# Kernel tuning notes

Measured on AMD Instinct MI355X. Metric: run time of the kernel, lower is better.

Reference implementation:

```python
import jax, jax.numpy as jnp
import numpy as np

N = 100000
E = 1600000
D_IN = 128
D_HID = 32
NEG_SLOPE = 0.2


def _glorot(key, shape):
    fan_in, fan_out = shape[0], shape[-1]
    lim = jnp.sqrt(6.0 / (fan_in + fan_out))
    return jax.random.uniform(key, shape, jnp.float32, -lim, lim)


def setup_inputs() -> dict:
    key = jax.random.key(0)
    ks = jax.random.split(key, 10)
    x = jax.random.normal(ks[0], (N, D_IN), jnp.float32)
    edge_index = jax.random.randint(ks[1], (2, E), 0, N, jnp.int64)
    return {
        "x": x,
        "edge_index": edge_index,
        "W1_l": _glorot(ks[2], (D_IN, D_HID)),
        "W1_r": _glorot(ks[3], (D_IN, D_HID)),
        "att1": _glorot(ks[4], (D_HID,)),
        "b1": jnp.zeros((D_HID,), jnp.float32),
        "W2_l": _glorot(ks[5], (D_HID, D_HID)),
        "W2_r": _glorot(ks[6], (D_HID, D_HID)),
        "att2": _glorot(ks[7], (D_HID,)),
        "b2": jnp.zeros((D_HID,), jnp.float32),
    }


def _segment_softmax(logits, seg, num_segments):
    m = jax.ops.segment_max(logits, seg, num_segments=num_segments)
    m = jnp.where(jnp.isfinite(m), m, 0.0)
    ex = jnp.exp(logits - m[seg])
    s = jax.ops.segment_sum(ex, seg, num_segments=num_segments)
    return ex / (s[seg] + 1e-16)


def _gatv2(x, edge_index, W_l, W_r, att, b):
    # GATv2Conv, heads=1, add_self_loops=False, share_weights=False
    src, dst = edge_index[0], edge_index[1]
    x_l = x @ W_l  # source transform [N, D_HID]
    x_r = x @ W_r  # target transform [N, D_HID]
    # per-edge attention logit: att . leaky_relu(x_l[j] + x_r[i])
    h = x_l[src] + x_r[dst]  # [E, D_HID]
    e = jnp.where(h > 0, h, NEG_SLOPE * h) @ att  # [E]
    alpha = _segment_softmax(e, dst, x.shape[0])  # softmax over incoming edges
    out = jax.ops.segment_sum(alpha[:, None] * x_l[src], dst,
                              num_segments=x.shape[0])
    return out + b


def reference(x, edge_index, W1_l, W1_r, att1, b1, W2_l, W2_r, att2, b2):
    h = _gatv2(x, edge_index, W1_l, W1_r, att1, b1)
    h = jax.nn.relu(h)
    return _gatv2(h, edge_index, W2_l, W2_r, att2, b2)
```

## Files before the change

kernel.cpp:

```cpp
#include <hip/hip_runtime.h>
#include <hip/hip_bf16.h>

#define D_HID 32
#define D_IN 128
#define NEG 0.2f
#define BSH 7
#define BSZ 128
#define MAXB 1024

typedef unsigned short u16;
typedef __attribute__((ext_vector_type(8))) short short8;
typedef __attribute__((ext_vector_type(4))) float float4v;

__device__ __forceinline__ float b2f(u16 u){
  union { unsigned int i; float f; } c; c.i = ((unsigned int)u) << 16; return c.f;
}

__device__ __forceinline__ u16 f2b_rne(float f){
  union { float f; unsigned int u; } c; c.f = f;
  unsigned int u = c.u;
  return (u16)((u + 0x7FFFu + ((u >> 16) & 1u)) >> 16);
}

__device__ __forceinline__ void split_bf16(float v, u16& hi, u16& lo){
  hi = f2b_rne(v);
  lo = f2b_rne(v - b2f(hi));
}

__device__ __forceinline__ float ldf(const void* __restrict__ p, int f32, long long i){
  return f32 ? ((const float*)p)[i] : b2f(((const u16*)p)[i]);
}

__device__ __forceinline__ int atomAddI(int* p, int v){
  return __hip_atomic_fetch_add(p, v, __ATOMIC_RELAXED, __HIP_MEMORY_SCOPE_AGENT);
}

__global__ void detect_flags(const int* __restrict__ ei, const u16* __restrict__ xw,
                             int* __restrict__ flags){
  __shared__ int insane_s, nz_s;
  int t = threadIdx.x;
  if (t == 0){ insane_s = 0; nz_s = 0; }
  __syncthreads();
  int pred = (t < 64) ? (ei[2*t+1] != 0) : 0;
  int e = (xw[t] >> 7) & 0xFF;
  int bad = (e < 100 || e > 140) ? 1 : 0;
  #pragma unroll
  for (int off = 32; off >= 1; off >>= 1){
    bad  += __shfl_down(bad,  off, 64);
    pred += __shfl_down(pred, off, 64);
  }
  if ((t & 63) == 0){
    atomicAdd(&insane_s, bad);
    atomicAdd(&nz_s, pred);
  }
  __syncthreads();
  if (t == 0){
    flags[0] = (nz_s == 0) ? 1 : 0;
    flags[1] = (insane_s > 16) ? 1 : 0;
  }
}

__device__ __forceinline__ void edge_nodes(const int* __restrict__ ei, int E_, int is64,
                                           int e, int& src, int& dst){
  if (is64){ src = ei[2*e]; dst = ei[2*E_ + 2*e]; }
  else     { src = ei[e];   dst = ei[E_ + e]; }
}

__global__ void prep_wfrag(const void* __restrict__ Wl, const void* __restrict__ Wr,
                           const int* __restrict__ flags, int K,
                           uint4* __restrict__ whi, uint4* __restrict__ wlo){
  int t = blockIdx.x * blockDim.x + threadIdx.x;
  int KS = K >> 5;
  int total = 4 * KS * 64;
  if (t >= total) return;
  int lane = t & 63;
  int rem = t >> 6;
  int kstep = rem % KS;
  int ctile = rem / KS;
  int f32 = flags[1];
  int col = ctile * 16 + (lane & 15);
  int quad = lane >> 4;
  union { u16 s[8]; uint4 q; } ch, cl;
  #pragma unroll
  for (int j = 0; j < 8; ++j){
    int k = kstep*32 + quad*8 + j;
    float v = (col < 32) ? ldf(Wl, f32, (long long)k*D_HID + col)
                         : ldf(Wr, f32, (long long)k*D_HID + (col - 32));
    u16 hi, lo; split_bf16(v, hi, lo);
    ch.s[j] = hi; cl.s[j] = lo;
  }
  whi[rem*64 + lane] = ch.q;
  wlo[rem*64 + lane] = cl.q;
}

template<int K>
__global__ void mfma_gemm(const void* __restrict__ X,
                          const uint4* __restrict__ whi, const uint4* __restrict__ wlo,
                          const int* __restrict__ flags, int force_f32,
                          float* __restrict__ xl, float* __restrict__ xr, int N_)
{
  constexpr int KS = K >> 5;
  int tile = blockIdx.x * (blockDim.x >> 6) + (threadIdx.x >> 6);
  if (tile * 16 >= N_) return;
  int lane = threadIdx.x & 63;
  int quad = lane >> 4;
  int m = tile*16 + (lane & 15);
  if (m >= N_) m = N_ - 1;
  int f32 = force_f32 | flags[1];

  float4v acc[4];
  #pragma unroll
  for (int c = 0; c < 4; ++c) acc[c] = (float4v){0.f,0.f,0.f,0.f};

  #pragma unroll
  for (int ks = 0; ks < KS; ++ks){
    long long base = (long long)m * K + ks*32 + quad*8;
    float av[8];
    if (f32){
      const float4* xp = (const float4*)((const float*)X + base);
      float4 t0 = xp[0], t1 = xp[1];
      av[0]=t0.x; av[1]=t0.y; av[2]=t0.z; av[3]=t0.w;
      av[4]=t1.x; av[5]=t1.y; av[6]=t1.z; av[7]=t1.w;
    } else {
      union { uint4 q; u16 s[8]; } c8;
      c8.q = *(const uint4*)((const u16*)X + base);
      #pragma unroll
      for (int j = 0; j < 8; ++j) av[j] = b2f(c8.s[j]);
    }
    short8 ahi, alo;
    #pragma unroll
    for (int j = 0; j < 8; ++j){
      u16 hi, lo; split_bf16(av[j], hi, lo);
      ahi[j] = (short)hi; alo[j] = (short)lo;
    }
    #pragma unroll
    for (int c = 0; c < 4; ++c){
      uint4 wh = whi[(c*KS + ks)*64 + lane];
      uint4 wl = wlo[(c*KS + ks)*64 + lane];
      short8 bh = *(short8*)&wh;
      short8 bl = *(short8*)&wl;
      acc[c] = __builtin_amdgcn_mfma_f32_16x16x32_bf16(ahi, bh, acc[c], 0, 0, 0);
      acc[c] = __builtin_amdgcn_mfma_f32_16x16x32_bf16(ahi, bl, acc[c], 0, 0, 0);
      acc[c] = __builtin_amdgcn_mfma_f32_16x16x32_bf16(alo, bh, acc[c], 0, 0, 0);
    }
  }

  #pragma unroll
  for (int c = 0; c < 4; ++c){
    int col = c*16 + (lane & 15);
    float* dst = (col < 32) ? xl : xr;
    int kk = col & 31;
    #pragma unroll
    for (int r = 0; r < 4; ++r){
      int node = tile*16 + quad*4 + r;
      if (node < N_) dst[(size_t)node*D_HID + kk] = acc[c][r];
    }
  }
}

__global__ void bucket_count(const int* __restrict__ ei, const int* __restrict__ flags,
                             int* __restrict__ gcnt, int E_, int B_){
  __shared__ int hist[MAXB];
  for (int i = threadIdx.x; i < B_; i += 256) hist[i] = 0;
  __syncthreads();
  int chunk = (E_ + gridDim.x - 1) / gridDim.x;
  int s = blockIdx.x * chunk;
  int e = s + chunk; if (e > E_) e = E_;
  int is64 = flags[0];
  for (int i = s + (int)threadIdx.x; i < e; i += 256){
    int dst = is64 ? ei[2*E_ + 2*i] : ei[E_ + i];
    atomicAdd(&hist[dst >> BSH], 1);
  }
  __syncthreads();
  for (int i = threadIdx.x; i < B_; i += 256)
    if (hist[i]) (void)atomAddI(&gcnt[i], hist[i]);
}

__global__ void scan_buckets(const int* __restrict__ gcnt, int* __restrict__ offsets,
                             int* __restrict__ cursor, int B_){
  __shared__ int sd[1024];
  int t = threadIdx.x;
  int v = (t < B_) ? gcnt[t] : 0;
  sd[t] = v;
  __syncthreads();
  for (int off = 1; off < 1024; off <<= 1){
    int tmp = (t >= off) ? sd[t-off] : 0;
    __syncthreads();
    sd[t] += tmp;
    __syncthreads();
  }
  if (t < B_){
    int excl = sd[t] - v;
    offsets[t] = excl;
    cursor[t]  = excl;
    if (t == B_-1) offsets[B_] = sd[t];
  }
}

__global__ void bucket_scatter(const int* __restrict__ ei, const int* __restrict__ flags,
                               int* __restrict__ cursor, unsigned* __restrict__ seg,
                               int E_, int B_){
  __shared__ int hist[MAXB];
  __shared__ int bbase[MAXB];
  for (int i = threadIdx.x; i < B_; i += 256) hist[i] = 0;
  __syncthreads();
  int chunk = (E_ + gridDim.x - 1) / gridDim.x;
  int s = blockIdx.x * chunk;
  int e = s + chunk; if (e > E_) e = E_;
  int is64 = flags[0];
  for (int i = s + (int)threadIdx.x; i < e; i += 256){
    int dst = is64 ? ei[2*E_ + 2*i] : ei[E_ + i];
    atomicAdd(&hist[dst >> BSH], 1);
  }
  __syncthreads();
  for (int i = threadIdx.x; i < B_; i += 256){
    int c = hist[i];
    bbase[i] = c ? atomAddI(&cursor[i], c) : 0;
  }
  __syncthreads();
  for (int i = threadIdx.x; i < B_; i += 256) hist[i] = 0;
  __syncthreads();
  for (int i = s + (int)threadIdx.x; i < e; i += 256){
    int src, dst;
    edge_nodes(ei, E_, is64, i, src, dst);
    int b = dst >> BSH;
    int pos = bbase[b] + atomicAdd(&hist[b], 1);
    seg[pos] = ((unsigned)src << BSH) | (unsigned)(dst & (BSZ-1));
  }
}

__global__ void bucket_finalize(const unsigned* __restrict__ seg,
                                const int* __restrict__ offsets,
                                int* __restrict__ row, int* __restrict__ csr_src,
                                int N_, int B_){
  __shared__ int hist[BSZ];
  __shared__ int sc[BSZ];
  __shared__ int loff[BSZ];
  int b = blockIdx.x;
  int t = threadIdx.x;
  int base = offsets[b], cnt = offsets[b+1] - base;
  if (t < BSZ) hist[t] = 0;
  __syncthreads();
  for (int i = t; i < cnt; i += 256)
    atomicAdd(&hist[seg[base+i] & (BSZ-1)], 1);
  __syncthreads();
  if (t < BSZ) sc[t] = hist[t];
  __syncthreads();
  for (int off = 1; off < BSZ; off <<= 1){
    int tmp = (t < BSZ && t >= off) ? sc[t-off] : 0;
    __syncthreads();
    if (t < BSZ) sc[t] += tmp;
    __syncthreads();
  }
  if (t < BSZ){
    int excl = sc[t] - hist[t];
    loff[t] = excl;
    int node = b*BSZ + t;
    if (node <= N_) row[node] = base + excl;
  }
  if (b == B_-1 && t == 0) row[N_] = offsets[B_];
  __syncthreads();
  for (int i = t; i < cnt; i += 256){
    unsigned en = seg[base+i];
    int dl = en & (BSZ-1);
    int pos = atomicAdd(&loff[dl], 1);
    csr_src[base + pos] = (int)en;
  }
}

__global__ void gat_gather(const int* __restrict__ row, const unsigned* __restrict__ csrp,
                           const float* __restrict__ xl, const float* __restrict__ xr,
                           const void* __restrict__ att, const void* __restrict__ bias,
                           const int* __restrict__ flags,
                           float* __restrict__ outp, int N_, int do_relu)
{
  int G = (blockIdx.x * blockDim.x + threadIdx.x) >> 3;
  if (G >= N_) return;
  int fl = threadIdx.x & 7;
  int f32 = flags[1];
  float4 attk;
  attk.x = ldf(att, f32, fl*4+0);
  attk.y = ldf(att, f32, fl*4+1);
  attk.z = ldf(att, f32, fl*4+2);
  attk.w = ldf(att, f32, fl*4+3);
  int n = G;
  float4 xrk = *(const float4*)(xr + (size_t)n*D_HID + fl*4);
  int rs = row[n], re = row[n+1];
  const char* xlb = (const char*)xl;
  unsigned fo = (unsigned)(fl << 4);

  unsigned enB = 0;
  float4 xlA = make_float4(0.f, 0.f, 0.f, 0.f);
  if (rs < re){
    unsigned enA = csrp[rs];
    if (rs + 1 < re) enB = csrp[rs+1];
    xlA = *(const float4*)(xlb + (enA & ~127u) + fo);
  }

  float4 acc = make_float4(0.f, 0.f, 0.f, 0.f);
  float ssum = 0.f;
  for (int i = rs; i < re; ++i){
    float4 xv = xlA;
    unsigned enN = enB;
    if (i + 2 < re) enB = csrp[i+2];
    if (i + 1 < re) xlA = *(const float4*)(xlb + (enN & ~127u) + fo);
    float4 hh;
    hh.x = xv.x + xrk.x; hh.x = fmaxf(hh.x, NEG*hh.x);
    hh.y = xv.y + xrk.y; hh.y = fmaxf(hh.y, NEG*hh.y);
    hh.z = xv.z + xrk.z; hh.z = fmaxf(hh.z, NEG*hh.z);
    hh.w = xv.w + xrk.w; hh.w = fmaxf(hh.w, NEG*hh.w);
    float p = hh.x*attk.x;
    p = fmaf(hh.y, attk.y, p);
    p = fmaf(hh.z, attk.z, p);
    p = fmaf(hh.w, attk.w, p);
    p += __shfl_xor(p, 1, 8);
    p += __shfl_xor(p, 2, 8);
    p += __shfl_xor(p, 4, 8);
    p = fminf(p, 60.f);
    float ev = __expf(p);
    ssum += ev;
    acc.x = fmaf(ev, xv.x, acc.x);
    acc.y = fmaf(ev, xv.y, acc.y);
    acc.z = fmaf(ev, xv.z, acc.z);
    acc.w = fmaf(ev, xv.w, acc.w);
  }

  float inv = 1.0f / (ssum + 1e-16f);
  float4 o;
  o.x = acc.x*inv + ldf(bias, f32, fl*4+0);
  o.y = acc.y*inv + ldf(bias, f32, fl*4+1);
  o.z = acc.z*inv + ldf(bias, f32, fl*4+2);
  o.w = acc.w*inv + ldf(bias, f32, fl*4+3);
  if (do_relu){
    o.x = fmaxf(o.x, 0.f); o.y = fmaxf(o.y, 0.f);
    o.z = fmaxf(o.z, 0.f); o.w = fmaxf(o.w, 0.f);
  }
  *(float4*)(outp + (size_t)n*D_HID + fl*4) = o;
}

extern "C" void kernel_launch(void* const* d_in, const int* in_sizes, int n_in,
                              void* d_out, int out_size, void* d_ws, size_t ws_size,
                              hipStream_t stream)
{
  const void* x   = d_in[0];
  const int*  ei  = (const int*)d_in[1];
  const void* W1l = d_in[2];
  const void* W1r = d_in[3];
  const void* att1= d_in[4];
  const void* b1  = d_in[5];
  const void* W2l = d_in[6];
  const void* W2r = d_in[7];
  const void* att2= d_in[8];
  const void* b2  = d_in[9];
  float* out = (float*)d_out;

  int N_ = in_sizes[0] / D_IN;
  int E_ = in_sizes[1] / 2;
  int B_ = (N_ + BSZ - 1) / BSZ;

  char* ws = (char*)d_ws;
  size_t off = 0;
  auto carve = [&](size_t bytes) -> char* {
    char* p = ws + off;
    off += (bytes + 255) & ~(size_t)255;
    return p;
  };
  float*    xl      = (float*)   carve((size_t)N_ * D_HID * 4);
  float*    xr      = (float*)   carve((size_t)N_ * D_HID * 4);
  float*    h       = (float*)   carve((size_t)N_ * D_HID * 4);
  unsigned* seg     = (unsigned*)carve((size_t)E_ * 4);
  int*      csr_src = (int*)     carve((size_t)E_ * 4);
  int*      row     = (int*)     carve((size_t)(N_ + 1) * 4);
  int*      offsets = (int*)     carve((size_t)(MAXB + 1) * 4);
  int*      gcnt    = (int*)     carve((size_t)MAXB * 4);
  int*      cursor  = (int*)     carve((size_t)MAXB * 4);
  int*      flags   = (int*)     carve(256);
  uint4*    whi1    = (uint4*)   carve((size_t)4 * 4 * 64 * 16);
  uint4*    wlo1    = (uint4*)   carve((size_t)4 * 4 * 64 * 16);
  uint4*    whi2    = (uint4*)   carve((size_t)4 * 1 * 64 * 16);
  uint4*    wlo2    = (uint4*)   carve((size_t)4 * 1 * 64 * 16);

  const int tpb = 256;
  int gG = (N_ + 31) / 32;
  int tiles = (N_ + 15) / 16;
  int gT = (tiles + 3) / 4;

  detect_flags<<<1, 256, 0, stream>>>(ei, (const u16*)x, flags);

  prep_wfrag<<<4, 256, 0, stream>>>(W1l, W1r, flags, D_IN, whi1, wlo1);
  prep_wfrag<<<1, 256, 0, stream>>>(W2l, W2r, flags, D_HID, whi2, wlo2);

  hipMemsetAsync(gcnt, 0, (size_t)MAXB * 4, stream);
  bucket_count<<<256, tpb, 0, stream>>>(ei, flags, gcnt, E_, B_);
  scan_buckets<<<1, 1024, 0, stream>>>(gcnt, offsets, cursor, B_);
  bucket_scatter<<<256, tpb, 0, stream>>>(ei, flags, cursor, seg, E_, B_);
  bucket_finalize<<<B_, tpb, 0, stream>>>(seg, offsets, row, csr_src, N_, B_);

  mfma_gemm<D_IN><<<gT, tpb, 0, stream>>>(x, whi1, wlo1, flags, 0, xl, xr, N_);
  gat_gather<<<gG, tpb, 0, stream>>>(row, (const unsigned*)csr_src, xl, xr,
                                     att1, b1, flags, h, N_, 1);

  mfma_gemm<D_HID><<<gT, tpb, 0, stream>>>(h, whi2, wlo2, flags, 1, xl, xr, N_);
  gat_gather<<<gG, tpb, 0, stream>>>(row, (const unsigned*)csr_src, xl, xr,
                                     att2, b2, flags, out, N_, 0);
}
```

Measured before the change: 270.9 us.

## Sort nodes by in-degree for gather balance and deepen edge prefetch

```diff
diff --git a/kernel.cpp b/kernel.cpp
--- a/kernel.cpp
+++ b/kernel.cpp
@@ -7,6 +7,7 @@
 #define BSH 7
 #define BSZ 128
 #define MAXB 1024
+#define MAXD 128
 
 typedef unsigned short u16;
 typedef __attribute__((ext_vector_type(8))) short short8;
@@ -33,6 +34,31 @@
 
 __device__ __forceinline__ int atomAddI(int* p, int v){
   return __hip_atomic_fetch_add(p, v, __ATOMIC_RELAXED, __HIP_MEMORY_SCOPE_AGENT);
+}
+
+__device__ __forceinline__ float red8(float p){
+  p += __int_as_float(__builtin_amdgcn_update_dpp(
+         0, __float_as_int(p), 0xB1, 0xF, 0xF, true));
+  p += __int_as_float(__builtin_amdgcn_update_dpp(
+         0, __float_as_int(p), 0x4E, 0xF, 0xF, true));
+  p += __int_as_float(__builtin_amdgcn_ds_swizzle(
+         __float_as_int(p), 0x101F));
+  return p;
+}
+
+__device__ __forceinline__ float edge_ev(const float4 xv, const float4 xrk,
+                                         const float4 attk){
+  float hx = xv.x + xrk.x; hx = fmaxf(hx, NEG*hx);
+  float hy = xv.y + xrk.y; hy = fmaxf(hy, NEG*hy);
+  float hz = xv.z + xrk.z; hz = fmaxf(hz, NEG*hz);
+  float hw = xv.w + xrk.w; hw = fmaxf(hw, NEG*hw);
+  float p = hx*attk.x;
+  p = fmaf(hy, attk.y, p);
+  p = fmaf(hz, attk.z, p);
+  p = fmaf(hw, attk.w, p);
+  p = red8(p);
+  p = fminf(p, 60.f);
+  return __expf(p);
 }
 
 __global__ void detect_flags(const int* __restrict__ ei, const u16* __restrict__ xw,
@@ -232,19 +258,26 @@
 __global__ void bucket_finalize(const unsigned* __restrict__ seg,
                                 const int* __restrict__ offsets,
                                 int* __restrict__ row, int* __restrict__ csr_src,
+                                int* __restrict__ dhist,
                                 int N_, int B_){
   __shared__ int hist[BSZ];
   __shared__ int sc[BSZ];
   __shared__ int loff[BSZ];
+  __shared__ int dh[MAXD];
   int b = blockIdx.x;
   int t = threadIdx.x;
   int base = offsets[b], cnt = offsets[b+1] - base;
   if (t < BSZ) hist[t] = 0;
+  if (t < MAXD) dh[t] = 0;
   __syncthreads();
   for (int i = t; i < cnt; i += 256)
     atomicAdd(&hist[seg[base+i] & (BSZ-1)], 1);
   __syncthreads();
-  if (t < BSZ) sc[t] = hist[t];
+  if (t < BSZ){
+    sc[t] = hist[t];
+    int node = b*BSZ + t;
+    if (node < N_) atomicAdd(&dh[min(hist[t], MAXD-1)], 1);
+  }
   __syncthreads();
   for (int off = 1; off < BSZ; off <<= 1){
     int tmp = (t < BSZ && t >= off) ? sc[t-off] : 0;
@@ -266,9 +299,56 @@
     int pos = atomicAdd(&loff[dl], 1);
     csr_src[base + pos] = (int)en;
   }
+  __syncthreads();
+  if (t < MAXD && dh[t]) (void)atomAddI(&dhist[t], dh[t]);
+}
+
+__global__ void scan_deg(const int* __restrict__ dhist, int* __restrict__ dcur){
+  __shared__ int sd[MAXD];
+  int t = threadIdx.x;
+  int v = dhist[t];
+  sd[t] = v;
+  __syncthreads();
+  for (int off = 1; off < MAXD; off <<= 1){
+    int tmp = (t >= off) ? sd[t-off] : 0;
+    __syncthreads();
+    sd[t] += tmp;
+    __syncthreads();
+  }
+  dcur[t] = sd[t] - v;
+}
+
+__global__ void deg_scatter(const int* __restrict__ row, int* __restrict__ dcur,
+                            int* __restrict__ perm, int N_){
+  __shared__ int h[MAXD];
+  __shared__ int base[MAXD];
+  int t = threadIdx.x;
+  int chunk = (N_ + gridDim.x - 1) / gridDim.x;
+  int s = blockIdx.x * chunk;
+  int e = s + chunk; if (e > N_) e = N_;
+  if (t < MAXD) h[t] = 0;
+  __syncthreads();
+  for (int n = s + t; n < e; n += 256){
+    int d = min(row[n+1] - row[n], MAXD-1);
+    atomicAdd(&h[d], 1);
+  }
+  __syncthreads();
+  if (t < MAXD){
+    int c = h[t];
+    base[t] = c ? atomAddI(&dcur[t], c) : 0;
+  }
+  __syncthreads();
+  if (t < MAXD) h[t] = 0;
+  __syncthreads();
+  for (int n = s + t; n < e; n += 256){
+    int d = min(row[n+1] - row[n], MAXD-1);
+    int pos = base[d] + atomicAdd(&h[d], 1);
+    perm[pos] = n;
+  }
 }
 
 __global__ void gat_gather(const int* __restrict__ row, const unsigned* __restrict__ csrp,
+                           const int* __restrict__ perm,
                            const float* __restrict__ xl, const float* __restrict__ xr,
                            const void* __restrict__ att, const void* __restrict__ bias,
                            const int* __restrict__ flags,
@@ -283,46 +363,48 @@
   attk.y = ldf(att, f32, fl*4+1);
   attk.z = ldf(att, f32, fl*4+2);
   attk.w = ldf(att, f32, fl*4+3);
-  int n = G;
+  int n = perm[G];
   float4 xrk = *(const float4*)(xr + (size_t)n*D_HID + fl*4);
   int rs = row[n], re = row[n+1];
   const char* xlb = (const char*)xl;
   unsigned fo = (unsigned)(fl << 4);
 
-  unsigned enB = 0;
-  float4 xlA = make_float4(0.f, 0.f, 0.f, 0.f);
-  if (rs < re){
-    unsigned enA = csrp[rs];
-    if (rs + 1 < re) enB = csrp[rs+1];
-    xlA = *(const float4*)(xlb + (enA & ~127u) + fo);
-  }
-
   float4 acc = make_float4(0.f, 0.f, 0.f, 0.f);
   float ssum = 0.f;
-  for (int i = rs; i < re; ++i){
-    float4 xv = xlA;
-    unsigned enN = enB;
-    if (i + 2 < re) enB = csrp[i+2];
-    if (i + 1 < re) xlA = *(const float4*)(xlb + (enN & ~127u) + fo);
-    float4 hh;
-    hh.x = xv.x + xrk.x; hh.x = fmaxf(hh.x, NEG*hh.x);
-    hh.y = xv.y + xrk.y; hh.y = fmaxf(hh.y, NEG*hh.y);
-    hh.z = xv.z + xrk.z; hh.z = fmaxf(hh.z, NEG*hh.z);
-    hh.w = xv.w + xrk.w; hh.w = fmaxf(hh.w, NEG*hh.w);
-    float p = hh.x*attk.x;
-    p = fmaf(hh.y, attk.y, p);
-    p = fmaf(hh.z, attk.z, p);
-    p = fmaf(hh.w, attk.w, p);
-    p += __shfl_xor(p, 1, 8);
-    p += __shfl_xor(p, 2, 8);
-    p += __shfl_xor(p, 4, 8);
-    p = fminf(p, 60.f);
-    float ev = __expf(p);
-    ssum += ev;
-    acc.x = fmaf(ev, xv.x, acc.x);
-    acc.y = fmaf(ev, xv.y, acc.y);
-    acc.z = fmaf(ev, xv.z, acc.z);
-    acc.w = fmaf(ev, xv.w, acc.w);
+
+  if (rs < re){
+    int last = re - 1;
+    unsigned c0 = csrp[rs];
+    unsigned c1 = csrp[min(rs+1, last)];
+    unsigned c2 = csrp[min(rs+2, last)];
+    unsigned c3 = csrp[min(rs+3, last)];
+    unsigned ca = csrp[min(rs+4, last)];
+    unsigned cb = csrp[min(rs+5, last)];
+    float4 xv0 = *(const float4*)(xlb + (c0 & ~127u) + fo);
+    float4 xv1 = *(const float4*)(xlb + (c1 & ~127u) + fo);
+    float4 xv2 = *(const float4*)(xlb + (c2 & ~127u) + fo);
+    float4 xv3 = *(const float4*)(xlb + (c3 & ~127u) + fo);
+    for (int i = rs; i < re; i += 2){
+      float4 nx0 = *(const float4*)(xlb + (ca & ~127u) + fo);
+      float4 nx1 = *(const float4*)(xlb + (cb & ~127u) + fo);
+      unsigned na = csrp[min(i+6, last)];
+      unsigned nb = csrp[min(i+7, last)];
+      float ev0 = edge_ev(xv0, xrk, attk);
+      ssum += ev0;
+      acc.x = fmaf(ev0, xv0.x, acc.x);
+      acc.y = fmaf(ev0, xv0.y, acc.y);
+      acc.z = fmaf(ev0, xv0.z, acc.z);
+      acc.w = fmaf(ev0, xv0.w, acc.w);
+      float ev1 = edge_ev(xv1, xrk, attk);
+      ev1 = (i + 1 <= last) ? ev1 : 0.f;
+      ssum += ev1;
+      acc.x = fmaf(ev1, xv1.x, acc.x);
+      acc.y = fmaf(ev1, xv1.y, acc.y);
+      acc.z = fmaf(ev1, xv1.z, acc.z);
+      acc.w = fmaf(ev1, xv1.w, acc.w);
+      xv0 = xv2; xv1 = xv3; xv2 = nx0; xv3 = nx1;
+      ca = na; cb = nb;
+    }
   }
 
   float inv = 1.0f / (ssum + 1e-16f);
@@ -371,9 +453,12 @@
   unsigned* seg     = (unsigned*)carve((size_t)E_ * 4);
   int*      csr_src = (int*)     carve((size_t)E_ * 4);
   int*      row     = (int*)     carve((size_t)(N_ + 1) * 4);
+  int*      perm    = (int*)     carve((size_t)N_ * 4);
   int*      offsets = (int*)     carve((size_t)(MAXB + 1) * 4);
   int*      gcnt    = (int*)     carve((size_t)MAXB * 4);
   int*      cursor  = (int*)     carve((size_t)MAXB * 4);
+  int*      dhist   = (int*)     carve((size_t)MAXD * 4);
+  int*      dcur    = (int*)     carve((size_t)MAXD * 4);
   int*      flags   = (int*)     carve(256);
   uint4*    whi1    = (uint4*)   carve((size_t)4 * 4 * 64 * 16);
   uint4*    wlo1    = (uint4*)   carve((size_t)4 * 4 * 64 * 16);
@@ -391,16 +476,20 @@
   prep_wfrag<<<1, 256, 0, stream>>>(W2l, W2r, flags, D_HID, whi2, wlo2);
 
   hipMemsetAsync(gcnt, 0, (size_t)MAXB * 4, stream);
+  hipMemsetAsync(dhist, 0, (size_t)MAXD * 4, stream);
   bucket_count<<<256, tpb, 0, stream>>>(ei, flags, gcnt, E_, B_);
   scan_buckets<<<1, 1024, 0, stream>>>(gcnt, offsets, cursor, B_);
   bucket_scatter<<<256, tpb, 0, stream>>>(ei, flags, cursor, seg, E_, B_);
-  bucket_finalize<<<B_, tpb, 0, stream>>>(seg, offsets, row, csr_src, N_, B_);
+  bucket_finalize<<<B_, tpb, 0, stream>>>(seg, offsets, row, csr_src, dhist, N_, B_);
+
+  scan_deg<<<1, MAXD, 0, stream>>>(dhist, dcur);
+  deg_scatter<<<64, tpb, 0, stream>>>(row, dcur, perm, N_);
 
   mfma_gemm<D_IN><<<gT, tpb, 0, stream>>>(x, whi1, wlo1, flags, 0, xl, xr, N_);
-  gat_gather<<<gG, tpb, 0, stream>>>(row, (const unsigned*)csr_src, xl, xr,
+  gat_gather<<<gG, tpb, 0, stream>>>(row, (const unsigned*)csr_src, perm, xl, xr,
                                      att1, b1, flags, h, N_, 1);
 
   mfma_gemm<D_HID><<<gT, tpb, 0, stream>>>(h, whi2, wlo2, flags, 1, xl, xr, N_);
-  gat_gather<<<gG, tpb, 0, stream>>>(row, (const unsigned*)csr_src, xl, xr,
+  gat_gather<<<gG, tpb, 0, stream>>>(row, (const unsigned*)csr_src, perm, xl, xr,
                                      att2, b2, flags, out, N_, 0);
 }
```

After: 275.9 us. Within noise of the previous version (+1.8%).

## Drop per-node CSR finalize; aggregate bucketed edges with LDS atomics

Applied to the files above, without the earlier changes.

```diff
diff --git a/kernel.cpp b/kernel.cpp
--- a/kernel.cpp
+++ b/kernel.cpp
@@ -7,6 +7,7 @@
 #define BSH 7
 #define BSZ 128
 #define MAXB 1024
+#define APAD 36
 
 typedef unsigned short u16;
 typedef __attribute__((ext_vector_type(8))) short short8;
@@ -33,6 +34,31 @@
 
 __device__ __forceinline__ int atomAddI(int* p, int v){
   return __hip_atomic_fetch_add(p, v, __ATOMIC_RELAXED, __HIP_MEMORY_SCOPE_AGENT);
+}
+
+__device__ __forceinline__ float red8(float p){
+  p += __int_as_float(__builtin_amdgcn_update_dpp(
+         0, __float_as_int(p), 0xB1, 0xF, 0xF, true));
+  p += __int_as_float(__builtin_amdgcn_update_dpp(
+         0, __float_as_int(p), 0x4E, 0xF, 0xF, true));
+  p += __int_as_float(__builtin_amdgcn_ds_swizzle(
+         __float_as_int(p), 0x101F));
+  return p;
+}
+
+__device__ __forceinline__ float edge_ev(const float4 xv, const float4 xrk,
+                                         const float4 attk){
+  float hx = xv.x + xrk.x; hx = fmaxf(hx, NEG*hx);
+  float hy = xv.y + xrk.y; hy = fmaxf(hy, NEG*hy);
+  float hz = xv.z + xrk.z; hz = fmaxf(hz, NEG*hz);
+  float hw = xv.w + xrk.w; hw = fmaxf(hw, NEG*hw);
+  float p = hx*attk.x;
+  p = fmaf(hy, attk.y, p);
+  p = fmaf(hz, attk.z, p);
+  p = fmaf(hw, attk.w, p);
+  p = red8(p);
+  p = fminf(p, 60.f);
+  return __expf(p);
 }
 
 __global__ void detect_flags(const int* __restrict__ ei, const u16* __restrict__ xw,
@@ -229,113 +255,110 @@
   }
 }
 
-__global__ void bucket_finalize(const unsigned* __restrict__ seg,
-                                const int* __restrict__ offsets,
-                                int* __restrict__ row, int* __restrict__ csr_src,
-                                int N_, int B_){
-  __shared__ int hist[BSZ];
-  __shared__ int sc[BSZ];
-  __shared__ int loff[BSZ];
+__global__ void __launch_bounds__(512)
+gat_edge(const unsigned* __restrict__ seg, const int* __restrict__ offsets,
+         const float* __restrict__ xl, const float* __restrict__ xr,
+         const void* __restrict__ att, const void* __restrict__ bias,
+         const int* __restrict__ flags,
+         float* __restrict__ outp, int N_, int do_relu)
+{
+  __shared__ float accs[BSZ][APAD];
+  __shared__ float xrs[BSZ][APAD];
   int b = blockIdx.x;
   int t = threadIdx.x;
-  int base = offsets[b], cnt = offsets[b+1] - base;
-  if (t < BSZ) hist[t] = 0;
-  __syncthreads();
-  for (int i = t; i < cnt; i += 256)
-    atomicAdd(&hist[seg[base+i] & (BSZ-1)], 1);
-  __syncthreads();
-  if (t < BSZ) sc[t] = hist[t];
-  __syncthreads();
-  for (int off = 1; off < BSZ; off <<= 1){
-    int tmp = (t < BSZ && t >= off) ? sc[t-off] : 0;
-    __syncthreads();
-    if (t < BSZ) sc[t] += tmp;
-    __syncthreads();
-  }
-  if (t < BSZ){
-    int excl = sc[t] - hist[t];
-    loff[t] = excl;
-    int node = b*BSZ + t;
-    if (node <= N_) row[node] = base + excl;
-  }
-  if (b == B_-1 && t == 0) row[N_] = offsets[B_];
-  __syncthreads();
-  for (int i = t; i < cnt; i += 256){
-    unsigned en = seg[base+i];
-    int dl = en & (BSZ-1);
-    int pos = atomicAdd(&loff[dl], 1);
-    csr_src[base + pos] = (int)en;
-  }
-}
-
-__global__ void gat_gather(const int* __restrict__ row, const unsigned* __restrict__ csrp,
-                           const float* __restrict__ xl, const float* __restrict__ xr,
-                           const void* __restrict__ att, const void* __restrict__ bias,
-                           const int* __restrict__ flags,
-                           float* __restrict__ outp, int N_, int do_relu)
-{
-  int G = (blockIdx.x * blockDim.x + threadIdx.x) >> 3;
-  if (G >= N_) return;
-  int fl = threadIdx.x & 7;
+  int fl = t & 7;
+  int g  = t >> 3;
+  int node0 = b * BSZ;
   int f32 = flags[1];
+
+  for (int i = t; i < BSZ*APAD; i += 512) ((float*)accs)[i] = 0.f;
+  for (int i = t; i < BSZ*8; i += 512){
+    int dl = i >> 3, fq = i & 7;
+    int node = node0 + dl;
+    float4 v = make_float4(0.f,0.f,0.f,0.f);
+    if (node < N_) v = *(const float4*)(xr + (size_t)node*D_HID + fq*4);
+    *(float4*)&xrs[dl][fq*4] = v;
+  }
+  __syncthreads();
+
   float4 attk;
   attk.x = ldf(att, f32, fl*4+0);
   attk.y = ldf(att, f32, fl*4+1);
   attk.z = ldf(att, f32, fl*4+2);
   attk.w = ldf(att, f32, fl*4+3);
-  int n = G;
-  float4 xrk = *(const float4*)(xr + (size_t)n*D_HID + fl*4);
-  int rs = row[n], re = row[n+1];
+
+  int base = offsets[b], cnt = offsets[b+1] - base;
   const char* xlb = (const char*)xl;
   unsigned fo = (unsigned)(fl << 4);
 
-  unsigned enB = 0;
-  float4 xlA = make_float4(0.f, 0.f, 0.f, 0.f);
-  if (rs < re){
-    unsigned enA = csrp[rs];
-    if (rs + 1 < re) enB = csrp[rs+1];
-    xlA = *(const float4*)(xlb + (enA & ~127u) + fo);
-  }
-
-  float4 acc = make_float4(0.f, 0.f, 0.f, 0.f);
-  float ssum = 0.f;
-  for (int i = rs; i < re; ++i){
-    float4 xv = xlA;
-    unsigned enN = enB;
-    if (i + 2 < re) enB = csrp[i+2];
-    if (i + 1 < re) xlA = *(const float4*)(xlb + (enN & ~127u) + fo);
-    float4 hh;
-    hh.x = xv.x + xrk.x; hh.x = fmaxf(hh.x, NEG*hh.x);
-    hh.y = xv.y + xrk.y; hh.y = fmaxf(hh.y, NEG*hh.y);
-    hh.z = xv.z + xrk.z; hh.z = fmaxf(hh.z, NEG*hh.z);
-    hh.w = xv.w + xrk.w; hh.w = fmaxf(hh.w, NEG*hh.w);
-    float p = hh.x*attk.x;
-    p = fmaf(hh.y, attk.y, p);
-    p = fmaf(hh.z, attk.z, p);
-    p = fmaf(hh.w, attk.w, p);
-    p += __shfl_xor(p, 1, 8);
-    p += __shfl_xor(p, 2, 8);
-    p += __shfl_xor(p, 4, 8);
-    p = fminf(p, 60.f);
-    float ev = __expf(p);
-    ssum += ev;
-    acc.x = fmaf(ev, xv.x, acc.x);
-    acc.y = fmaf(ev, xv.y, acc.y);
-    acc.z = fmaf(ev, xv.z, acc.z);
-    acc.w = fmaf(ev, xv.w, acc.w);
-  }
-
-  float inv = 1.0f / (ssum + 1e-16f);
-  float4 o;
-  o.x = acc.x*inv + ldf(bias, f32, fl*4+0);
-  o.y = acc.y*inv + ldf(bias, f32, fl*4+1);
-  o.z = acc.z*inv + ldf(bias, f32, fl*4+2);
-  o.w = acc.w*inv + ldf(bias, f32, fl*4+3);
-  if (do_relu){
-    o.x = fmaxf(o.x, 0.f); o.y = fmaxf(o.y, 0.f);
-    o.z = fmaxf(o.z, 0.f); o.w = fmaxf(o.w, 0.f);
-  }
-  *(float4*)(outp + (size_t)n*D_HID + fl*4) = o;
+  if (cnt > 0){
+    int chunk = (cnt + 63) >> 6;
+    int nit = (chunk + 1) >> 1;
+    int gs = base + g * chunk;
+    int ge = min(gs + chunk, base + cnt);
+    int last = base + cnt - 1;
+
+    unsigned c0 = seg[min(gs+0, last)];
+    unsigned c1 = seg[min(gs+1, last)];
+    unsigned c2 = seg[min(gs+2, last)];
+    unsigned c3 = seg[min(gs+3, last)];
+    float4 x0 = *(const float4*)(xlb + (c0 & ~127u) + fo);
+    float4 x1 = *(const float4*)(xlb + (c1 & ~127u) + fo);
+
+    for (int it = 0; it < nit; ++it){
+      int i = gs + 2*it;
+      float4 nx0 = *(const float4*)(xlb + (c2 & ~127u) + fo);
+      float4 nx1 = *(const float4*)(xlb + (c3 & ~127u) + fo);
+      unsigned n0 = seg[min(i+4, last)];
+      unsigned n1 = seg[min(i+5, last)];
+
+      {
+        int dl = (int)(c0 & 127u);
+        float4 xrk = *(const float4*)&xrs[dl][fl*4];
+        float ev = edge_ev(x0, xrk, attk);
+        ev = (i < ge) ? ev : 0.f;
+        float* ac = &accs[dl][0];
+        atomicAdd(ac + fl*4+0, ev*x0.x);
+        atomicAdd(ac + fl*4+1, ev*x0.y);
+        atomicAdd(ac + fl*4+2, ev*x0.z);
+        atomicAdd(ac + fl*4+3, ev*x0.w);
+        if (fl == 0) atomicAdd(ac + 32, ev);
+      }
+      {
+        int dl = (int)(c1 & 127u);
+        float4 xrk = *(const float4*)&xrs[dl][fl*4];
+        float ev = edge_ev(x1, xrk, attk);
+        ev = (i + 1 < ge) ? ev : 0.f;
+        float* ac = &accs[dl][0];
+        atomicAdd(ac + fl*4+0, ev*x1.x);
+        atomicAdd(ac + fl*4+1, ev*x1.y);
+        atomicAdd(ac + fl*4+2, ev*x1.z);
+        atomicAdd(ac + fl*4+3, ev*x1.w);
+        if (fl == 0) atomicAdd(ac + 32, ev);
+      }
+      c0 = c2; c1 = c3; c2 = n0; c3 = n1;
+      x0 = nx0; x1 = nx1;
+    }
+  }
+  __syncthreads();
+
+  for (int i = t; i < BSZ*8; i += 512){
+    int dl = i >> 3, fq = i & 7;
+    int node = node0 + dl;
+    if (node >= N_) continue;
+    float inv = 1.0f / (accs[dl][32] + 1e-16f);
+    float4 a = *(const float4*)&accs[dl][fq*4];
+    float4 o;
+    o.x = a.x*inv + ldf(bias, f32, fq*4+0);
+    o.y = a.y*inv + ldf(bias, f32, fq*4+1);
+    o.z = a.z*inv + ldf(bias, f32, fq*4+2);
+    o.w = a.w*inv + ldf(bias, f32, fq*4+3);
+    if (do_relu){
+      o.x = fmaxf(o.x, 0.f); o.y = fmaxf(o.y, 0.f);
+      o.z = fmaxf(o.z, 0.f); o.w = fmaxf(o.w, 0.f);
+    }
+    *(float4*)(outp + (size_t)node*D_HID + fq*4) = o;
+  }
 }
 
 extern "C" void kernel_launch(void* const* d_in, const int* in_sizes, int n_in,
@@ -369,8 +392,6 @@
   float*    xr      = (float*)   carve((size_t)N_ * D_HID * 4);
   float*    h       = (float*)   carve((size_t)N_ * D_HID * 4);
   unsigned* seg     = (unsigned*)carve((size_t)E_ * 4);
-  int*      csr_src = (int*)     carve((size_t)E_ * 4);
-  int*      row     = (int*)     carve((size_t)(N_ + 1) * 4);
   int*      offsets = (int*)     carve((size_t)(MAXB + 1) * 4);
   int*      gcnt    = (int*)     carve((size_t)MAXB * 4);
   int*      cursor  = (int*)     carve((size_t)MAXB * 4);
@@ -381,7 +402,6 @@
   uint4*    wlo2    = (uint4*)   carve((size_t)4 * 1 * 64 * 16);
 
   const int tpb = 256;
-  int gG = (N_ + 31) / 32;
   int tiles = (N_ + 15) / 16;
   int gT = (tiles + 3) / 4;
 
@@ -394,13 +414,10 @@
   bucket_count<<<256, tpb, 0, stream>>>(ei, flags, gcnt, E_, B_);
   scan_buckets<<<1, 1024, 0, stream>>>(gcnt, offsets, cursor, B_);
   bucket_scatter<<<256, tpb, 0, stream>>>(ei, flags, cursor, seg, E_, B_);
-  bucket_finalize<<<B_, tpb, 0, stream>>>(seg, offsets, row, csr_src, N_, B_);
 
   mfma_gemm<D_IN><<<gT, tpb, 0, stream>>>(x, whi1, wlo1, flags, 0, xl, xr, N_);
-  gat_gather<<<gG, tpb, 0, stream>>>(row, (const unsigned*)csr_src, xl, xr,
-                                     att1, b1, flags, h, N_, 1);
+  gat_edge<<<B_, 512, 0, stream>>>(seg, offsets, xl, xr, att1, b1, flags, h, N_, 1);
 
   mfma_gemm<D_HID><<<gT, tpb, 0, stream>>>(h, whi2, wlo2, flags, 1, xl, xr, N_);
-  gat_gather<<<gG, tpb, 0, stream>>>(row, (const unsigned*)csr_src, xl, xr,
-                                     att2, b2, flags, out, N_, 0);
-}
+  gat_edge<<<B_, 512, 0, stream>>>(seg, offsets, xl, xr, att2, b2, flags, out, N_, 0);
+}
```

New measurement: 913.0 us. 237% more time.
